# Kernel optimization log

Hardware: AMD Instinct MI355X
Metric: run time of the kernel (lower is better)

Reference implementation:

```python
import jax, jax.numpy as jnp
import numpy as np

B, E, C_IN, C_OUT, BLOCKS = 4, 50000, 32, 64, 2
EPS = 1e-5


def setup_inputs() -> dict:
    key = jax.random.key(0)
    k = jax.random.split(key, 7)
    fe = jax.random.normal(k[0], (B, C_IN, E), dtype=jnp.float32)
    edge_index = jax.random.randint(k[1], (B, E, 4), 0, E, dtype=jnp.int32)
    s1 = 1.0 / np.sqrt(C_IN * 5)
    s2 = 1.0 / np.sqrt(C_OUT * 5)
    conv1_w = jax.random.uniform(k[2], (C_OUT, C_IN, 5), jnp.float32, -s1, s1)
    conv1_b = jax.random.uniform(k[3], (C_OUT,), jnp.float32, -s1, s1)
    conv2_w = jax.random.uniform(k[4], (BLOCKS, C_OUT, C_OUT, 5), jnp.float32, -s2, s2)
    conv2_b = jax.random.uniform(k[5], (BLOCKS, C_OUT), jnp.float32, -s2, s2)
    return {"fe": fe, "edge_index": edge_index, "conv1_w": conv1_w,
            "conv1_b": conv1_b, "conv2_w": conv2_w, "conv2_b": conv2_b}


def _mesh_conv(x, edge_index, W, b):
    # x: [B, C, E]; edge_index: [B, E, 4]; W: [O, C, 5]; b: [O]
    nb = jax.vmap(lambda f, i: f[:, i])(x, edge_index)  # [B, C, E, 4]
    n1, n2, n3, n4 = nb[..., 0], nb[..., 1], nb[..., 2], nb[..., 3]
    # MeshCNN symmetric neighborhood functions -> [B, C, E, 5]
    feats = jnp.stack([x, n1 + n3, n2 + n4,
                       jnp.abs(n1 - n3), jnp.abs(n2 - n4)], axis=-1)
    # Conv2d with kernel (1,5) over the symmetric axis
    return jnp.einsum('bces,ocs->boe', feats, W) + b[None, :, None]


def _instance_norm(x):
    # InstanceNorm2d (affine=False): normalize each (b, c) over spatial E
    m = jnp.mean(x, axis=-1, keepdims=True)
    v = jnp.var(x, axis=-1, keepdims=True)
    return (x - m) * jax.lax.rsqrt(v + EPS)


def reference(fe, edge_index, conv1_w, conv1_b, conv2_w, conv2_b):
    x1 = jax.nn.relu(_instance_norm(_mesh_conv(fe, edge_index, conv1_w, conv1_b)))
    for i in range(BLOCKS):
        x2 = _mesh_conv(x1, edge_index, conv2_w[i], conv2_b[i])
        x2 = jax.nn.relu(_instance_norm(x2) + x1)
        x1 = x2
    return x1  # [B, C_OUT, E]; pool=0 -> before_pool is None
```

## Files before the change

kernel.cpp:

```cpp
#include <hip/hip_runtime.h>
#include <math.h>

#define B_    4
#define E_    50000
#define CIN_  32
#define CO_   64
#define EPS_  1e-5f
#define NBLK_ 196
#define NT_   ((E_ + 63) / 64)

typedef __attribute__((ext_vector_type(8))) short  s16x8;
typedef __attribute__((ext_vector_type(4))) float  f32x4;
typedef unsigned short u16;

__device__ __forceinline__ u16 f2bf(float f) {
    unsigned u = __builtin_bit_cast(unsigned, f);
    u += 0x7fffu + ((u >> 16) & 1u);
    return (u16)(u >> 16);
}
__device__ __forceinline__ float bf2f(u16 h) {
    return __builtin_bit_cast(float, (unsigned)h << 16);
}


__global__ __launch_bounds__(256) void k_transpose_in(
    const float* __restrict__ fe, u16* __restrict__ fet)
{
    __shared__ float t[CIN_][65];
    const int b = blockIdx.y;
    const int e0 = blockIdx.x * 64;
    for (int idx = threadIdx.x; idx < CIN_ * 64; idx += 256) {
        int c = idx >> 6, el = idx & 63, e = e0 + el;
        t[c][el] = (e < E_) ? fe[((size_t)b * CIN_ + c) * E_ + e] : 0.f;
    }
    __syncthreads();
    for (int idx = threadIdx.x; idx < 64 * CIN_; idx += 256) {
        int el = idx >> 5, c = idx & 31, e = e0 + el;
        if (e < E_) fet[((size_t)b * E_ + e) * CIN_ + c] = f2bf(t[c][el]);
    }
}

template<int C>
__global__ __launch_bounds__(256, 3) void k_conv_mfma(
    const u16* __restrict__ xt, const int* __restrict__ ei,
    const float* __restrict__ W, const float* __restrict__ bias,
    u16* __restrict__ y, float* __restrict__ st)
{
    constexpr int K  = 5 * C;
    constexpr int KF = K / 32;
    constexpr int SL = ((K / 8) + 7) & ~7;
    constexpr int CH = C / 4;
    constexpr int YP = 72;

    __shared__ alignas(16) u16 smem[64 * SL * 8];
    __shared__ alignas(16) u16 ytile[64 * YP];

    const int id  = blockIdx.x;
    const int xcd = id & 7;
    const int b   = xcd >> 1;
    const int j   = ((id >> 3) << 1) | (xcd & 1);

    const int t = threadIdx.x;
    const int w = t >> 6;
    const int l = t & 63;

    constexpr int WELEM = CO_ * K;
    for (int i4 = t; i4 < WELEM / 4; i4 += 256) {
        const float4 v = reinterpret_cast<const float4*>(W)[i4];
        const float vv[4] = {v.x, v.y, v.z, v.w};
#pragma unroll
        for (int jj = 0; jj < 4; ++jj) {
            const int idx = i4 * 4 + jj;
            const int o   = idx / (C * 5);
            const int rem = idx - o * (C * 5);
            const int c   = rem / 5;
            const int s   = rem - c * 5;
            const int el  = o * K + s * C + c;
            const int adr = (((el >> 3) ^ (o & 7)) << 3) | (el & 7);
            smem[adr] = f2bf(vv[jj]);
        }
    }
    __syncthreads();

    s16x8 bw[KF];
    const int o = w * 16 + (l & 15);
#pragma unroll
    for (int kf = 0; kf < KF; ++kf) {
        const int el  = o * K + kf * 32 + (l >> 4) * 8;
        const int adr = (((el >> 3) ^ (o & 7)) << 3);
        bw[kf] = *reinterpret_cast<const s16x8*>(smem + adr);
    }
    const float bv = bias[o];
    float sacc = 0.f, ssacc = 0.f;
    __syncthreads();

    const u16* xb = xt + (size_t)b * E_ * C;
    u16* ybase = y + (size_t)b * E_ * CO_;

#pragma unroll 1
    for (int tt = j; tt < NT_; tt += NBLK_) {
        const int e0 = tt * 64;

        {
            const int m = t >> 2;
            const int q = t & 3;
            const int e = e0 + m;
            const bool valid = e < E_;
            int4 nb;
            if (valid) nb = *reinterpret_cast<const int4*>(ei + ((size_t)b * E_ + e) * 4);
            else { nb.x = 0; nb.y = 0; nb.z = 0; nb.w = 0; }
            const u16* re = xb + (size_t)e    * C;
            const u16* r1 = xb + (size_t)nb.x * C;
            const u16* r2 = xb + (size_t)nb.y * C;
            const u16* r3 = xb + (size_t)nb.z * C;
            const u16* r4 = xb + (size_t)nb.w * C;
#pragma unroll
            for (int hh = 0; hh < CH / 8; ++hh) {
                const int cb = q * CH + hh * 8;
                s16x8 fo[5];
                if (valid) {
                    const s16x8 xe = *reinterpret_cast<const s16x8*>(re + cb);
                    const s16x8 a1 = *reinterpret_cast<const s16x8*>(r1 + cb);
                    const s16x8 a2 = *reinterpret_cast<const s16x8*>(r2 + cb);
                    const s16x8 a3 = *reinterpret_cast<const s16x8*>(r3 + cb);
                    const s16x8 a4 = *reinterpret_cast<const s16x8*>(r4 + cb);
                    fo[0] = xe;
#pragma unroll
                    for (int d = 0; d < 8; ++d) {
                        const float v1 = bf2f((u16)a1[d]);
                        const float v2 = bf2f((u16)a2[d]);
                        const float v3 = bf2f((u16)a3[d]);
                        const float v4 = bf2f((u16)a4[d]);
                        fo[1][d] = (short)f2bf(v1 + v3);
                        fo[2][d] = (short)f2bf(v2 + v4);
                        fo[3][d] = (short)f2bf(fabsf(v1 - v3));
                        fo[4][d] = (short)f2bf(fabsf(v2 - v4));
                    }
                } else {
#pragma unroll
                    for (int s = 0; s < 5; ++s) fo[s] = s16x8{0,0,0,0,0,0,0,0};
                }
#pragma unroll
                for (int s = 0; s < 5; ++s) {
                    const int in_slot = (s * C + cb) >> 3;
                    const int adr = (m * SL + (in_slot ^ (m & 7))) << 3;
                    *reinterpret_cast<s16x8*>(smem + adr) = fo[s];
                }
            }
        }
        __syncthreads();

#pragma unroll
        for (int mf = 0; mf < 4; ++mf) {
            f32x4 acc = f32x4{0.f, 0.f, 0.f, 0.f};
            const int ma = mf * 16 + (l & 15);
#pragma unroll
            for (int kf = 0; kf < KF; ++kf) {
                const int slot = kf * 4 + (l >> 4);
                const int adr  = (ma * SL + (slot ^ (ma & 7))) << 3;
                const s16x8 a  = *reinterpret_cast<const s16x8*>(smem + adr);
                acc = __builtin_amdgcn_mfma_f32_16x16x32_bf16(a, bw[kf], acc, 0, 0, 0);
            }
#pragma unroll
            for (int r = 0; r < 4; ++r) {
                const int m = mf * 16 + (l >> 4) * 4 + r;
                const float v = acc[r] + bv;
                ytile[m * YP + o] = f2bf(v);
                if (e0 + m < E_) { sacc += v; ssacc += v * v; }
            }
        }
        __syncthreads();

        for (int idx = t; idx < 512; idx += 256) {
            const int row = idx >> 3, c8 = idx & 7;
            if (e0 + row < E_)
                *reinterpret_cast<s16x8*>(ybase + (size_t)(e0 + row) * CO_ + c8 * 8) =
                    *reinterpret_cast<const s16x8*>(ytile + row * YP + c8 * 8);
        }
        __syncthreads();
    }

    sacc  += __shfl_xor(sacc, 16);  ssacc += __shfl_xor(ssacc, 16);
    sacc  += __shfl_xor(sacc, 32);  ssacc += __shfl_xor(ssacc, 32);
    if (l < 16) {
        atomicAdd(&st[(b * CO_ + o) * 2 + 0], sacc);
        atomicAdd(&st[(b * CO_ + o) * 2 + 1], ssacc);
    }
}

template<bool ADD>
__global__ __launch_bounds__(256) void k_norm(
    const u16* __restrict__ y, const float* __restrict__ st,
    u16* __restrict__ x1)
{
    constexpr float invE = 1.f / E_;
    const size_t total8 = (size_t)B_ * E_ * CO_ / 8;
    for (size_t i8 = (size_t)blockIdx.x * 256 + threadIdx.x; i8 < total8;
         i8 += (size_t)gridDim.x * 256) {
        const size_t i = i8 * 8;
        const int b = (int)(i / ((size_t)E_ * CO_));
        const int c = (int)(i & 63);
        const s16x8 yv = reinterpret_cast<const s16x8*>(y)[i8];
        s16x8 xv;
        if (ADD) xv = reinterpret_cast<const s16x8*>(x1)[i8];
        const float4* stp = reinterpret_cast<const float4*>(st + ((size_t)b * CO_ + c) * 2);
        s16x8 ov;
#pragma unroll
        for (int d2 = 0; d2 < 4; ++d2) {
            const float4 s2 = stp[d2];
            const float m0 = s2.x * invE, v0 = s2.y * invE - m0 * m0;
            const float m1 = s2.z * invE, v1 = s2.w * invE - m1 * m1;
            float a0 = (bf2f((u16)yv[d2*2])   - m0) * rsqrtf(v0 + EPS_);
            float a1 = (bf2f((u16)yv[d2*2+1]) - m1) * rsqrtf(v1 + EPS_);
            if (ADD) { a0 += bf2f((u16)xv[d2*2]); a1 += bf2f((u16)xv[d2*2+1]); }
            ov[d2*2]   = (short)f2bf(fmaxf(a0, 0.f));
            ov[d2*2+1] = (short)f2bf(fmaxf(a1, 0.f));
        }
        reinterpret_cast<s16x8*>(x1)[i8] = ov;
    }
}

__global__ __launch_bounds__(256) void k_norm_t(
    const u16* __restrict__ y, const float* __restrict__ st,
    const u16* __restrict__ x1, float* __restrict__ out)
{
    __shared__ float tt[CO_][65];
    constexpr float invE = 1.f / E_;
    const int b  = blockIdx.y;
    const int e0 = blockIdx.x * 64;
    const int t  = threadIdx.x;
    for (int idx = t; idx < 512; idx += 256) {
        const int el = idx >> 3, c = (idx & 7) * 8;
        const int e  = e0 + el;
        if (e < E_) {
            const size_t base = ((size_t)b * E_ + e) * CO_ + c;
            const s16x8 yv = *reinterpret_cast<const s16x8*>(y  + base);
            const s16x8 xv = *reinterpret_cast<const s16x8*>(x1 + base);
            const float4* stp = reinterpret_cast<const float4*>(st + ((size_t)b * CO_ + c) * 2);
#pragma unroll
            for (int d2 = 0; d2 < 4; ++d2) {
                const float4 s2 = stp[d2];
                const float m0 = s2.x * invE, v0 = s2.y * invE - m0 * m0;
                const float m1 = s2.z * invE, v1 = s2.w * invE - m1 * m1;
                const float a0 = (bf2f((u16)yv[d2*2])   - m0) * rsqrtf(v0 + EPS_) + bf2f((u16)xv[d2*2]);
                const float a1 = (bf2f((u16)yv[d2*2+1]) - m1) * rsqrtf(v1 + EPS_) + bf2f((u16)xv[d2*2+1]);
                tt[c + d2*2][el]     = fmaxf(a0, 0.f);
                tt[c + d2*2 + 1][el] = fmaxf(a1, 0.f);
            }
        }
    }
    __syncthreads();
    for (int idx = t; idx < 1024; idx += 256) {
        const int c = idx >> 4, seg = idx & 15;
        const int e = e0 + seg * 4;
        float* op = out + ((size_t)b * CO_ + c) * E_;
        if (e + 3 < E_) {
            float4 v = {tt[c][seg*4], tt[c][seg*4+1], tt[c][seg*4+2], tt[c][seg*4+3]};
            *reinterpret_cast<float4*>(op + e) = v;
        } else {
#pragma unroll
            for (int k2 = 0; k2 < 4; ++k2)
                if (e + k2 < E_) op[e + k2] = tt[c][seg*4 + k2];
        }
    }
}

extern "C" void kernel_launch(void* const* d_in, const int* in_sizes, int n_in,
                              void* d_out, int out_size, void* d_ws, size_t ws_size,
                              hipStream_t stream)
{
    const float* fe = (const float*)d_in[0];
    const int*   ei = (const int*)  d_in[1];
    const float* W1 = (const float*)d_in[2];
    const float* b1 = (const float*)d_in[3];
    const float* W2 = (const float*)d_in[4];
    const float* b2 = (const float*)d_in[5];

    u16*   x1  = (u16*)d_ws;
    u16*   y   = x1 + (size_t)B_ * E_ * CO_;
    float* st  = (float*)(y + (size_t)B_ * E_ * CO_);
    u16*   fet = x1;
    float* out = (float*)d_out;

    const dim3 blk(256);
    const dim3 gT(NT_, B_);
    const dim3 gC(NBLK_ * B_);

    k_transpose_in<<<gT, blk, 0, stream>>>(fe, fet);

    hipMemsetAsync(st, 0, B_ * CO_ * 2 * sizeof(float), stream);
    k_conv_mfma<CIN_><<<gC, blk, 0, stream>>>(fet, ei, W1, b1, y, st);
    k_norm<false><<<2048, blk, 0, stream>>>(y, st, x1);

    hipMemsetAsync(st, 0, B_ * CO_ * 2 * sizeof(float), stream);
    k_conv_mfma<CO_><<<gC, blk, 0, stream>>>(x1, ei, W2, b2, y, st);
    k_norm<true><<<2048, blk, 0, stream>>>(y, st, x1);

    hipMemsetAsync(st, 0, B_ * CO_ * 2 * sizeof(float), stream);
    k_conv_mfma<CO_><<<gC, blk, 0, stream>>>(x1, ei, W2 + (size_t)CO_ * CO_ * 5,
                                             b2 + CO_, y, st);
    k_norm_t<<<gT, blk, 0, stream>>>(y, st, x1, out);
}
```

Baseline: 256.2 us.

## Software-pipeline neighbor gathers across tiles and fold stat zeroing into transpose

Inside the conv kernel, the edge-index load and the neighbor-row gathers for the next tile are now issued into registers before the MFMA phase of the current tile, so global-load latency overlaps with compute. The ytile writeback is deferred to the next iteration, which removes one __syncthreads per tile. The three hipMemsetAsync calls are replaced by having the transpose kernel zero three separate stat buffers, one per conv. This costs extra registers for the prefetched gathers, which under launch_bounds(256,3) could lead to spills.

```diff
diff --git a/kernel.cpp b/kernel.cpp
--- a/kernel.cpp
+++ b/kernel.cpp
@@ -24,8 +24,11 @@
 
 
 __global__ __launch_bounds__(256) void k_transpose_in(
-    const float* __restrict__ fe, u16* __restrict__ fet)
-{
+    const float* __restrict__ fe, u16* __restrict__ fet, float* __restrict__ st)
+{
+    if (blockIdx.x == 0 && blockIdx.y == 0)
+        for (int i = threadIdx.x; i < 3 * 512; i += 256) st[i] = 0.f;
+
     __shared__ float t[CIN_][65];
     const int b = blockIdx.y;
     const int e0 = blockIdx.x * 64;
@@ -40,6 +43,37 @@
     }
 }
 
+__device__ __forceinline__ int4 load_ei_row(const int* __restrict__ ei_b,
+                                            int tile, int m)
+{
+    const int e = tile * 64 + m;
+    if (e < E_) return *reinterpret_cast<const int4*>(ei_b + (size_t)e * 4);
+    int4 z; z.x = 0; z.y = 0; z.z = 0; z.w = 0; return z;
+}
+
+template<int C, int NG>
+__device__ __forceinline__ void issue_gathers(
+    const u16* __restrict__ xb, int e0, int m, int q, const int4 nb,
+    s16x8 (&G)[5][NG])
+{
+    constexpr int CH = C / 4;
+    const int e = (e0 + m < E_) ? (e0 + m) : 0;
+    const u16* r0 = xb + (size_t)e    * C;
+    const u16* r1 = xb + (size_t)nb.x * C;
+    const u16* r2 = xb + (size_t)nb.y * C;
+    const u16* r3 = xb + (size_t)nb.z * C;
+    const u16* r4 = xb + (size_t)nb.w * C;
+#pragma unroll
+    for (int g = 0; g < NG; ++g) {
+        const int cb = q * CH + g * 8;
+        G[0][g] = *reinterpret_cast<const s16x8*>(r0 + cb);
+        G[1][g] = *reinterpret_cast<const s16x8*>(r1 + cb);
+        G[2][g] = *reinterpret_cast<const s16x8*>(r2 + cb);
+        G[3][g] = *reinterpret_cast<const s16x8*>(r3 + cb);
+        G[4][g] = *reinterpret_cast<const s16x8*>(r4 + cb);
+    }
+}
+
 template<int C>
 __global__ __launch_bounds__(256, 3) void k_conv_mfma(
     const u16* __restrict__ xt, const int* __restrict__ ei,
@@ -50,6 +84,7 @@
     constexpr int KF = K / 32;
     constexpr int SL = ((K / 8) + 7) & ~7;
     constexpr int CH = C / 4;
+    constexpr int NG = CH / 8;
     constexpr int YP = 72;
 
     __shared__ alignas(16) u16 smem[64 * SL * 8];
@@ -96,58 +131,67 @@
 
     const u16* xb = xt + (size_t)b * E_ * C;
     u16* ybase = y + (size_t)b * E_ * CO_;
+    const int* ei_b = ei + (size_t)b * E_ * 4;
+
+    const int m = t >> 2;
+    const int q = t & 3;
+
+    s16x8 G[5][NG];
+    {
+        const int4 nb0 = load_ei_row(ei_b, j, m);
+        issue_gathers<C, NG>(xb, j * 64, m, q, nb0, G);
+    }
+    int e0_prev = -1;
 
 #pragma unroll 1
     for (int tt = j; tt < NT_; tt += NBLK_) {
         const int e0 = tt * 64;
-
-        {
-            const int m = t >> 2;
-            const int q = t & 3;
-            const int e = e0 + m;
-            const bool valid = e < E_;
-            int4 nb;
-            if (valid) nb = *reinterpret_cast<const int4*>(ei + ((size_t)b * E_ + e) * 4);
-            else { nb.x = 0; nb.y = 0; nb.z = 0; nb.w = 0; }
-            const u16* re = xb + (size_t)e    * C;
-            const u16* r1 = xb + (size_t)nb.x * C;
-            const u16* r2 = xb + (size_t)nb.y * C;
-            const u16* r3 = xb + (size_t)nb.z * C;
-            const u16* r4 = xb + (size_t)nb.w * C;
-#pragma unroll
-            for (int hh = 0; hh < CH / 8; ++hh) {
-                const int cb = q * CH + hh * 8;
-                s16x8 fo[5];
-                if (valid) {
-                    const s16x8 xe = *reinterpret_cast<const s16x8*>(re + cb);
-                    const s16x8 a1 = *reinterpret_cast<const s16x8*>(r1 + cb);
-                    const s16x8 a2 = *reinterpret_cast<const s16x8*>(r2 + cb);
-                    const s16x8 a3 = *reinterpret_cast<const s16x8*>(r3 + cb);
-                    const s16x8 a4 = *reinterpret_cast<const s16x8*>(r4 + cb);
-                    fo[0] = xe;
-#pragma unroll
-                    for (int d = 0; d < 8; ++d) {
-                        const float v1 = bf2f((u16)a1[d]);
-                        const float v2 = bf2f((u16)a2[d]);
-                        const float v3 = bf2f((u16)a3[d]);
-                        const float v4 = bf2f((u16)a4[d]);
-                        fo[1][d] = (short)f2bf(v1 + v3);
-                        fo[2][d] = (short)f2bf(v2 + v4);
-                        fo[3][d] = (short)f2bf(fabsf(v1 - v3));
-                        fo[4][d] = (short)f2bf(fabsf(v2 - v4));
-                    }
-                } else {
-#pragma unroll
-                    for (int s = 0; s < 5; ++s) fo[s] = s16x8{0,0,0,0,0,0,0,0};
+        const int tn = tt + NBLK_;
+        const bool valid = (e0 + m) < E_;
+
+        int4 nb_n;
+        if (tn < NT_) nb_n = load_ei_row(ei_b, tn, m);
+
+#pragma unroll
+        for (int g = 0; g < NG; ++g) {
+            const int cb = q * CH + g * 8;
+            s16x8 fo[5];
+            if (valid) {
+                fo[0] = G[0][g];
+#pragma unroll
+                for (int d = 0; d < 8; ++d) {
+                    const float v1 = bf2f((u16)G[1][g][d]);
+                    const float v2 = bf2f((u16)G[2][g][d]);
+                    const float v3 = bf2f((u16)G[3][g][d]);
+                    const float v4 = bf2f((u16)G[4][g][d]);
+                    fo[1][d] = (short)f2bf(v1 + v3);
+                    fo[2][d] = (short)f2bf(v2 + v4);
+                    fo[3][d] = (short)f2bf(fabsf(v1 - v3));
+                    fo[4][d] = (short)f2bf(fabsf(v2 - v4));
                 }
-#pragma unroll
-                for (int s = 0; s < 5; ++s) {
-                    const int in_slot = (s * C + cb) >> 3;
-                    const int adr = (m * SL + (in_slot ^ (m & 7))) << 3;
-                    *reinterpret_cast<s16x8*>(smem + adr) = fo[s];
-                }
-            }
-        }
+            } else {
+#pragma unroll
+                for (int s = 0; s < 5; ++s) fo[s] = s16x8{0,0,0,0,0,0,0,0};
+            }
+#pragma unroll
+            for (int s = 0; s < 5; ++s) {
+                const int in_slot = (s * C + cb) >> 3;
+                const int adr = (m * SL + (in_slot ^ (m & 7))) << 3;
+                *reinterpret_cast<s16x8*>(smem + adr) = fo[s];
+            }
+        }
+
+        if (e0_prev >= 0) {
+            for (int idx = t; idx < 512; idx += 256) {
+                const int row = idx >> 3, c8 = idx & 7;
+                if (e0_prev + row < E_)
+                    *reinterpret_cast<s16x8*>(ybase + (size_t)(e0_prev + row) * CO_ + c8 * 8) =
+                        *reinterpret_cast<const s16x8*>(ytile + row * YP + c8 * 8);
+            }
+        }
+
+        if (tn < NT_) issue_gathers<C, NG>(xb, tn * 64, m, q, nb_n, G);
+
         __syncthreads();
 
 #pragma unroll
@@ -163,21 +207,23 @@
             }
 #pragma unroll
             for (int r = 0; r < 4; ++r) {
-                const int m = mf * 16 + (l >> 4) * 4 + r;
+                const int mm = mf * 16 + (l >> 4) * 4 + r;
                 const float v = acc[r] + bv;
-                ytile[m * YP + o] = f2bf(v);
-                if (e0 + m < E_) { sacc += v; ssacc += v * v; }
+                ytile[mm * YP + o] = f2bf(v);
+                if (e0 + mm < E_) { sacc += v; ssacc += v * v; }
             }
         }
         __syncthreads();
-
+        e0_prev = e0;
+    }
+
+    if (e0_prev >= 0) {
         for (int idx = t; idx < 512; idx += 256) {
             const int row = idx >> 3, c8 = idx & 7;
-            if (e0 + row < E_)
-                *reinterpret_cast<s16x8*>(ybase + (size_t)(e0 + row) * CO_ + c8 * 8) =
+            if (e0_prev + row < E_)
+                *reinterpret_cast<s16x8*>(ybase + (size_t)(e0_prev + row) * CO_ + c8 * 8) =
                     *reinterpret_cast<const s16x8*>(ytile + row * YP + c8 * 8);
         }
-        __syncthreads();
     }
 
     sacc  += __shfl_xor(sacc, 16);  ssacc += __shfl_xor(ssacc, 16);
@@ -286,18 +332,15 @@
     const dim3 gT(NT_, B_);
     const dim3 gC(NBLK_ * B_);
 
-    k_transpose_in<<<gT, blk, 0, stream>>>(fe, fet);
-
-    hipMemsetAsync(st, 0, B_ * CO_ * 2 * sizeof(float), stream);
+    k_transpose_in<<<gT, blk, 0, stream>>>(fe, fet, st);
+
     k_conv_mfma<CIN_><<<gC, blk, 0, stream>>>(fet, ei, W1, b1, y, st);
     k_norm<false><<<2048, blk, 0, stream>>>(y, st, x1);
 
-    hipMemsetAsync(st, 0, B_ * CO_ * 2 * sizeof(float), stream);
-    k_conv_mfma<CO_><<<gC, blk, 0, stream>>>(x1, ei, W2, b2, y, st);
-    k_norm<true><<<2048, blk, 0, stream>>>(y, st, x1);
-
-    hipMemsetAsync(st, 0, B_ * CO_ * 2 * sizeof(float), stream);
+    k_conv_mfma<CO_><<<gC, blk, 0, stream>>>(x1, ei, W2, b2, y, st + 512);
+    k_norm<true><<<2048, blk, 0, stream>>>(y, st + 512, x1);
+
     k_conv_mfma<CO_><<<gC, blk, 0, stream>>>(x1, ei, W2 + (size_t)CO_ * CO_ * 5,
-                                             b2 + CO_, y, st);
-    k_norm_t<<<gT, blk, 0, stream>>>(y, st, x1, out);
-}
+                                             b2 + CO_, y, st + 1024);
+    k_norm_t<<<gT, blk, 0, stream>>>(y, st + 1024, x1, out);
+}
```

After: 296.9 us. 1.16x slower.

## Shrink conv edge tile for wide layer and fold stats zeroing into transpose

Applied to the files above, without the earlier changes.

The conv kernel is now templated on edges per tile. The 64-channel layers use 32-edge tiles with one 8-channel vector per builder thread, and weights are staged into shared memory in two passes so the smaller buffer still holds them. The smaller shared footprint allows a launch bound of 4 blocks per CU instead of 3. The three hipMemsetAsync calls are replaced by having the transpose kernel zero three separate stats buffers, removing extra stream operations. The trade-off is twice as many tile iterations, with more barriers per edge, in the wide layers; since the grid is only a few blocks per CU, the extra occupancy may go unused.

```diff
diff --git a/kernel.cpp b/kernel.cpp
--- a/kernel.cpp
+++ b/kernel.cpp
@@ -24,8 +24,11 @@
 
 
 __global__ __launch_bounds__(256) void k_transpose_in(
-    const float* __restrict__ fe, u16* __restrict__ fet)
-{
+    const float* __restrict__ fe, u16* __restrict__ fet, float* __restrict__ st)
+{
+    if (blockIdx.x == 0 && blockIdx.y == 0)
+        for (int i = threadIdx.x; i < 3 * 512; i += 256) st[i] = 0.f;
+
     __shared__ float t[CIN_][65];
     const int b = blockIdx.y;
     const int e0 = blockIdx.x * 64;
@@ -40,20 +43,31 @@
     }
 }
 
-template<int C>
-__global__ __launch_bounds__(256, 3) void k_conv_mfma(
+template<int C, int EDG>
+__global__ __launch_bounds__(256, 4) void k_conv_mfma(
     const u16* __restrict__ xt, const int* __restrict__ ei,
     const float* __restrict__ W, const float* __restrict__ bias,
     u16* __restrict__ y, float* __restrict__ st)
 {
-    constexpr int K  = 5 * C;
-    constexpr int KF = K / 32;
-    constexpr int SL = ((K / 8) + 7) & ~7;
-    constexpr int CH = C / 4;
-    constexpr int YP = 72;
-
-    __shared__ alignas(16) u16 smem[64 * SL * 8];
-    __shared__ alignas(16) u16 ytile[64 * YP];
+    constexpr int K   = 5 * C;
+    constexpr int KF  = K / 32;
+    constexpr int SL  = ((K / 8) + 7) & ~7;
+    constexpr int TPE = 256 / EDG;
+    constexpr int LG  = (TPE == 4) ? 2 : 3;
+    static_assert(C / TPE == 8, "one s16x8 per builder thread");
+    constexpr int MF  = EDG / 16;
+    constexpr int NTt = (E_ + EDG - 1) / EDG;
+    constexpr int YP  = 72;
+
+    constexpr int SMEM_U16 = EDG * SL * 8;
+    constexpr int NPASS = (CO_ * K > SMEM_U16) ? 2 : 1;
+    constexpr int WR    = CO_ / NPASS;
+    static_assert(WR * K <= SMEM_U16, "W staging pass must fit in smem");
+    static_assert(WR % 8 == 0, "row-swizzle needs 8-row alignment");
+    static_assert((WR * K) % 4 == 0, "float4 staging");
+
+    __shared__ alignas(16) u16 smem[SMEM_U16];
+    __shared__ alignas(16) u16 ytile[EDG * YP];
 
     const int id  = blockIdx.x;
     const int xcd = id & 7;
@@ -64,94 +78,98 @@
     const int w = t >> 6;
     const int l = t & 63;
 
-    constexpr int WELEM = CO_ * K;
-    for (int i4 = t; i4 < WELEM / 4; i4 += 256) {
-        const float4 v = reinterpret_cast<const float4*>(W)[i4];
-        const float vv[4] = {v.x, v.y, v.z, v.w};
-#pragma unroll
-        for (int jj = 0; jj < 4; ++jj) {
-            const int idx = i4 * 4 + jj;
-            const int o   = idx / (C * 5);
-            const int rem = idx - o * (C * 5);
-            const int c   = rem / 5;
-            const int s   = rem - c * 5;
-            const int el  = o * K + s * C + c;
-            const int adr = (((el >> 3) ^ (o & 7)) << 3) | (el & 7);
-            smem[adr] = f2bf(vv[jj]);
-        }
-    }
-    __syncthreads();
-
     s16x8 bw[KF];
     const int o = w * 16 + (l & 15);
 #pragma unroll
-    for (int kf = 0; kf < KF; ++kf) {
-        const int el  = o * K + kf * 32 + (l >> 4) * 8;
-        const int adr = (((el >> 3) ^ (o & 7)) << 3);
-        bw[kf] = *reinterpret_cast<const s16x8*>(smem + adr);
+    for (int p = 0; p < NPASS; ++p) {
+        const float4* Wp = reinterpret_cast<const float4*>(W + (size_t)p * WR * K);
+        for (int i4 = t; i4 < WR * K / 4; i4 += 256) {
+            const float4 v = Wp[i4];
+            const float vv[4] = {v.x, v.y, v.z, v.w};
+#pragma unroll
+            for (int jj = 0; jj < 4; ++jj) {
+                const int idx = i4 * 4 + jj;
+                const int ol  = idx / (C * 5);
+                const int rem = idx - ol * (C * 5);
+                const int c   = rem / 5;
+                const int s   = rem - c * 5;
+                const int el  = ol * K + s * C + c;
+                const int adr = (((el >> 3) ^ (ol & 7)) << 3) | (el & 7);
+                smem[adr] = f2bf(vv[jj]);
+            }
+        }
+        __syncthreads();
+        if (o >= p * WR && o < (p + 1) * WR) {
+            const int lo = o - p * WR;
+#pragma unroll
+            for (int kf = 0; kf < KF; ++kf) {
+                const int el  = lo * K + kf * 32 + (l >> 4) * 8;
+                const int adr = (((el >> 3) ^ (lo & 7)) << 3);
+                bw[kf] = *reinterpret_cast<const s16x8*>(smem + adr);
+            }
+        }
+        __syncthreads();
     }
     const float bv = bias[o];
     float sacc = 0.f, ssacc = 0.f;
-    __syncthreads();
 
     const u16* xb = xt + (size_t)b * E_ * C;
     u16* ybase = y + (size_t)b * E_ * CO_;
+    const int* ei_b = ei + (size_t)b * E_ * 4;
+
+    const int m = t >> LG;
+    const int q = t & (TPE - 1);
+    const int cb = q * 8;
 
 #pragma unroll 1
-    for (int tt = j; tt < NT_; tt += NBLK_) {
-        const int e0 = tt * 64;
+    for (int tt = j; tt < NTt; tt += NBLK_) {
+        const int e0 = tt * EDG;
+        const int e  = e0 + m;
+        const bool valid = e < E_;
 
         {
-            const int m = t >> 2;
-            const int q = t & 3;
-            const int e = e0 + m;
-            const bool valid = e < E_;
             int4 nb;
-            if (valid) nb = *reinterpret_cast<const int4*>(ei + ((size_t)b * E_ + e) * 4);
+            if (valid) nb = *reinterpret_cast<const int4*>(ei_b + (size_t)e * 4);
             else { nb.x = 0; nb.y = 0; nb.z = 0; nb.w = 0; }
-            const u16* re = xb + (size_t)e    * C;
-            const u16* r1 = xb + (size_t)nb.x * C;
-            const u16* r2 = xb + (size_t)nb.y * C;
-            const u16* r3 = xb + (size_t)nb.z * C;
-            const u16* r4 = xb + (size_t)nb.w * C;
-#pragma unroll
-            for (int hh = 0; hh < CH / 8; ++hh) {
-                const int cb = q * CH + hh * 8;
-                s16x8 fo[5];
-                if (valid) {
-                    const s16x8 xe = *reinterpret_cast<const s16x8*>(re + cb);
-                    const s16x8 a1 = *reinterpret_cast<const s16x8*>(r1 + cb);
-                    const s16x8 a2 = *reinterpret_cast<const s16x8*>(r2 + cb);
-                    const s16x8 a3 = *reinterpret_cast<const s16x8*>(r3 + cb);
-                    const s16x8 a4 = *reinterpret_cast<const s16x8*>(r4 + cb);
-                    fo[0] = xe;
-#pragma unroll
-                    for (int d = 0; d < 8; ++d) {
-                        const float v1 = bf2f((u16)a1[d]);
-                        const float v2 = bf2f((u16)a2[d]);
-                        const float v3 = bf2f((u16)a3[d]);
-                        const float v4 = bf2f((u16)a4[d]);
-                        fo[1][d] = (short)f2bf(v1 + v3);
-                        fo[2][d] = (short)f2bf(v2 + v4);
-                        fo[3][d] = (short)f2bf(fabsf(v1 - v3));
-                        fo[4][d] = (short)f2bf(fabsf(v2 - v4));
-                    }
-                } else {
-#pragma unroll
-                    for (int s = 0; s < 5; ++s) fo[s] = s16x8{0,0,0,0,0,0,0,0};
+            s16x8 fo[5];
+            if (valid) {
+                const u16* re = xb + (size_t)e    * C;
+                const u16* r1 = xb + (size_t)nb.x * C;
+                const u16* r2 = xb + (size_t)nb.y * C;
+                const u16* r3 = xb + (size_t)nb.z * C;
+                const u16* r4 = xb + (size_t)nb.w * C;
+                const s16x8 xe = *reinterpret_cast<const s16x8*>(re + cb);
+                const s16x8 a1 = *reinterpret_cast<const s16x8*>(r1 + cb);
+                const s16x8 a2 = *reinterpret_cast<const s16x8*>(r2 + cb);
+                const s16x8 a3 = *reinterpret_cast<const s16x8*>(r3 + cb);
+                const s16x8 a4 = *reinterpret_cast<const s16x8*>(r4 + cb);
+                fo[0] = xe;
+#pragma unroll
+                for (int d = 0; d < 8; ++d) {
+                    const float v1 = bf2f((u16)a1[d]);
+                    const float v2 = bf2f((u16)a2[d]);
+                    const float v3 = bf2f((u16)a3[d]);
+                    const float v4 = bf2f((u16)a4[d]);
+                    fo[1][d] = (short)f2bf(v1 + v3);
+                    fo[2][d] = (short)f2bf(v2 + v4);
+                    fo[3][d] = (short)f2bf(fabsf(v1 - v3));
+                    fo[4][d] = (short)f2bf(fabsf(v2 - v4));
                 }
-#pragma unroll
-                for (int s = 0; s < 5; ++s) {
-                    const int in_slot = (s * C + cb) >> 3;
-                    const int adr = (m * SL + (in_slot ^ (m & 7))) << 3;
-                    *reinterpret_cast<s16x8*>(smem + adr) = fo[s];
-                }
-            }
-        }
-        __syncthreads();
-
-#pragma unroll
-        for (int mf = 0; mf < 4; ++mf) {
+            } else {
+#pragma unroll
+                for (int s = 0; s < 5; ++s) fo[s] = s16x8{0,0,0,0,0,0,0,0};
+            }
+#pragma unroll
+            for (int s = 0; s < 5; ++s) {
+                const int in_slot = (s * C + cb) >> 3;
+                const int adr = (m * SL + (in_slot ^ (m & 7))) << 3;
+                *reinterpret_cast<s16x8*>(smem + adr) = fo[s];
+            }
+        }
+        __syncthreads();
+
+#pragma unroll
+        for (int mf = 0; mf < MF; ++mf) {
             f32x4 acc = f32x4{0.f, 0.f, 0.f, 0.f};
             const int ma = mf * 16 + (l & 15);
 #pragma unroll
@@ -163,15 +181,15 @@
             }
 #pragma unroll
             for (int r = 0; r < 4; ++r) {
-                const int m = mf * 16 + (l >> 4) * 4 + r;
+                const int mm = mf * 16 + (l >> 4) * 4 + r;
                 const float v = acc[r] + bv;
-                ytile[m * YP + o] = f2bf(v);
-                if (e0 + m < E_) { sacc += v; ssacc += v * v; }
-            }
-        }
-        __syncthreads();
-
-        for (int idx = t; idx < 512; idx += 256) {
+                ytile[mm * YP + o] = f2bf(v);
+                if (e0 + mm < E_) { sacc += v; ssacc += v * v; }
+            }
+        }
+        __syncthreads();
+
+        for (int idx = t; idx < EDG * 8; idx += 256) {
             const int row = idx >> 3, c8 = idx & 7;
             if (e0 + row < E_)
                 *reinterpret_cast<s16x8*>(ybase + (size_t)(e0 + row) * CO_ + c8 * 8) =
@@ -286,18 +304,15 @@
     const dim3 gT(NT_, B_);
     const dim3 gC(NBLK_ * B_);
 
-    k_transpose_in<<<gT, blk, 0, stream>>>(fe, fet);
-
-    hipMemsetAsync(st, 0, B_ * CO_ * 2 * sizeof(float), stream);
-    k_conv_mfma<CIN_><<<gC, blk, 0, stream>>>(fet, ei, W1, b1, y, st);
+    k_transpose_in<<<gT, blk, 0, stream>>>(fe, fet, st);
+
+    k_conv_mfma<CIN_, 64><<<gC, blk, 0, stream>>>(fet, ei, W1, b1, y, st);
     k_norm<false><<<2048, blk, 0, stream>>>(y, st, x1);
 
-    hipMemsetAsync(st, 0, B_ * CO_ * 2 * sizeof(float), stream);
-    k_conv_mfma<CO_><<<gC, blk, 0, stream>>>(x1, ei, W2, b2, y, st);
-    k_norm<true><<<2048, blk, 0, stream>>>(y, st, x1);
-
-    hipMemsetAsync(st, 0, B_ * CO_ * 2 * sizeof(float), stream);
-    k_conv_mfma<CO_><<<gC, blk, 0, stream>>>(x1, ei, W2 + (size_t)CO_ * CO_ * 5,
-                                             b2 + CO_, y, st);
-    k_norm_t<<<gT, blk, 0, stream>>>(y, st, x1, out);
-}
+    k_conv_mfma<CO_, 32><<<gC, blk, 0, stream>>>(x1, ei, W2, b2, y, st + 512);
+    k_norm<true><<<2048, blk, 0, stream>>>(y, st + 512, x1);
+
+    k_conv_mfma<CO_, 32><<<gC, blk, 0, stream>>>(x1, ei, W2 + (size_t)CO_ * CO_ * 5,
+                                                 b2 + CO_, y, st + 1024);
+    k_norm_t<<<gT, blk, 0, stream>>>(y, st + 1024, x1, out);
+}
```

Result: faster. 240.0 us (-6.3%).
